# Kernel optimization log

Hardware: AMD Instinct MI355X
Metric: run time of the kernel (lower is better)

Reference implementation:

```python
import jax, jax.numpy as jnp
import numpy as np

B, T, E, WIN, OC, VOCAB = 256, 2048, 128, 5, 128, 50000


def setup_inputs() -> dict:
    key = jax.random.key(0)
    k1, k2, k3, k4, k5, k6 = jax.random.split(key, 6)
    return {
        "x": jax.random.randint(k1, (B, T), 0, VOCAB + 1, dtype=jnp.int32),
        "emb_table": jax.random.normal(k2, (VOCAB + 1, E), dtype=jnp.float32),
        "att_w": jax.random.normal(k3, (WIN, E), dtype=jnp.float32) * 0.05,
        "att_b": jax.random.normal(k4, (1,), dtype=jnp.float32),
        "cnn_w": jax.random.normal(k5, (OC, E), dtype=jnp.float32) * 0.05,
        "cnn_b": jax.random.normal(k6, (OC,), dtype=jnp.float32),
    }


def reference(x, emb_table, att_w, att_b, cnn_w, cnn_b):
    win = att_w.shape[0]
    pad = (win - 1) // 2
    embed = emb_table[x]                                   # [B, T, E]
    x_pad = jnp.pad(embed, ((0, 0), (pad, pad), (0, 0)))
    T_ = embed.shape[1]
    # Sliding-window dot product over full embed dim (the degenerate Conv2d)
    s = jnp.zeros(embed.shape[:2], dtype=embed.dtype)      # [B, T]
    for k in range(win):
        s = s + jnp.einsum('bte,e->bt', x_pad[:, k:k + T_, :], att_w[k])
    scores = jax.nn.sigmoid(s + att_b[0])                  # [B, T]
    gated = embed * scores[:, :, None]                     # [B, T, E]
    feat = jnp.tanh(jnp.einsum('bte,oe->bto', gated, cnn_w) + cnn_b)  # [B, T, OC]
    out = jnp.max(feat, axis=1)                            # [B, OC] (maxpool over seq)
    return out[:, :, None, None]                           # [B, OC, 1, 1]
```

## Files before the change

kernel.cpp:

```cpp
#include <hip/hip_runtime.h>
#include <hip/hip_bf16.h>
#include <math.h>

#define B_   256
#define T_   2048
#define E_   128
#define WIN_ 5
#define PAD_ 2
#define OC_  128
#define VOCAB_MAX 50000
#define VOCAB1 50001
#define TT   64
#define REAL_ROWS (TT + WIN_ - 1)
#define ROWS 80
#define ASTR 136
#define DSTR 132
#define VROWS 64
#define BT   256

typedef __attribute__((ext_vector_type(8))) short short8;
typedef __attribute__((ext_vector_type(4))) float floatx4;
typedef __attribute__((ext_vector_type(4))) unsigned uintx4;

static __device__ __forceinline__ short f2bf(float f) {
    union { __hip_bfloat16 h; short s; } u;
    u.h = __float2bfloat16(f);
    return u.s;
}

__device__ __forceinline__ void atomicMaxFloat(float* addr, float v) {
    if (v >= 0.0f) atomicMax((int*)addr, __float_as_int(v));
    else           atomicMin((unsigned int*)addr, __float_as_uint(v));
}

__launch_bounds__(256, 3)
__global__ void build_tables(const float* __restrict__ emb,
                             const float* __restrict__ cnn_w,
                             const float* __restrict__ att_w,
                             unsigned char* __restrict__ D8,
                             float* __restrict__ r,
                             float* __restrict__ rs,
                             float* __restrict__ out) {
    __shared__ __align__(16) short sh_a[VROWS * ASTR];
    __shared__ __align__(16) float sh_df[VROWS * DSTR];
    __shared__ float sh_inv[VROWS];

    const int tid  = threadIdx.x;
    const int lane = tid & 63;
    const int w    = tid >> 6;
    const int l15  = lane & 15;
    const int quad = lane >> 4;
    const int v0   = blockIdx.x * VROWS;

    if (blockIdx.x < (B_ * OC_) / 256)
        out[blockIdx.x * 256 + tid] = -INFINITY;

    #pragma unroll
    for (int t = 0; t < 8; t++) {
        int i   = t * 256 + tid;
        int row = i >> 5, c4 = i & 31;
        int vr  = v0 + row; if (vr > VOCAB_MAX) vr = VOCAB_MAX;
        float4 v = *(const float4*)(emb + (size_t)vr * E_ + c4 * 4);
        short4 o; o.x = f2bf(v.x); o.y = f2bf(v.y); o.z = f2bf(v.z); o.w = f2bf(v.w);
        *(short4*)(&sh_a[row * ASTR + c4 * 4]) = o;
    }

    short8 Bf[2][4];
    #pragma unroll
    for (int j = 0; j < 2; j++)
        #pragma unroll
        for (int ks = 0; ks < 4; ks++) {
            const float4* p = (const float4*)(cnn_w + (size_t)(w * 32 + j * 16 + l15) * E_ + ks * 32 + quad * 8);
            float4 p0 = p[0], p1 = p[1];
            Bf[j][ks] = (short8){ f2bf(p0.x), f2bf(p0.y), f2bf(p0.z), f2bf(p0.w),
                                  f2bf(p1.x), f2bf(p1.y), f2bf(p1.z), f2bf(p1.w) };
        }

    short8 Ba[4];
    #pragma unroll
    for (int ks = 0; ks < 4; ks++) {
        short8 v = (short8){0,0,0,0,0,0,0,0};
        if (l15 < WIN_) {
            const float4* p = (const float4*)(att_w + (size_t)l15 * E_ + ks * 32 + quad * 8);
            float4 p0 = p[0], p1 = p[1];
            v = (short8){ f2bf(p0.x), f2bf(p0.y), f2bf(p0.z), f2bf(p0.w),
                          f2bf(p1.x), f2bf(p1.y), f2bf(p1.z), f2bf(p1.w) };
        }
        Ba[ks] = v;
    }
    __syncthreads();

    #pragma unroll
    for (int mt = 0; mt < 4; mt++) {
        short8 a[4];
        #pragma unroll
        for (int ks = 0; ks < 4; ks++)
            a[ks] = *(const short8*)(&sh_a[(mt * 16 + l15) * ASTR + ks * 32 + quad * 8]);
        #pragma unroll
        for (int j = 0; j < 2; j++) {
            floatx4 acc = (floatx4){0.f, 0.f, 0.f, 0.f};
            #pragma unroll
            for (int ks = 0; ks < 4; ks++)
                acc = __builtin_amdgcn_mfma_f32_16x16x32_bf16(a[ks], Bf[j][ks], acc, 0, 0, 0);
            #pragma unroll
            for (int rr = 0; rr < 4; rr++)
                sh_df[(mt * 16 + quad * 4 + rr) * DSTR + w * 32 + j * 16 + l15] = acc[rr];
        }
    }

    {
        short8 a[4];
        #pragma unroll
        for (int ks = 0; ks < 4; ks++)
            a[ks] = *(const short8*)(&sh_a[(w * 16 + l15) * ASTR + ks * 32 + quad * 8]);
        floatx4 acc = (floatx4){0.f, 0.f, 0.f, 0.f};
        #pragma unroll
        for (int ks = 0; ks < 4; ks++)
            acc = __builtin_amdgcn_mfma_f32_16x16x32_bf16(a[ks], Ba[ks], acc, 0, 0, 0);
        if (l15 < 8) {
            #pragma unroll
            for (int rr = 0; rr < 4; rr++) {
                int v = v0 + w * 16 + quad * 4 + rr;
                if (v <= VOCAB_MAX) r[(size_t)v * 8 + l15] = acc[rr];
            }
        }
    }
    __syncthreads();

    {
        int row = tid >> 2, seg = tid & 3;
        const float4* p = (const float4*)(&sh_df[row * DSTR + seg * 32]);
        float m = 0.f;
        #pragma unroll
        for (int k = 0; k < 8; k++) {
            float4 v = p[k];
            m = fmaxf(m, fmaxf(fmaxf(fabsf(v.x), fabsf(v.y)), fmaxf(fabsf(v.z), fabsf(v.w))));
        }
        m = fmaxf(m, __shfl_xor(m, 1));
        m = fmaxf(m, __shfl_xor(m, 2));
        if (seg == 0) {
            sh_inv[row] = (m > 0.f) ? 127.f / m : 0.f;
            int v = v0 + row;
            if (v <= VOCAB_MAX) rs[v] = m * (1.f / 127.f);
        }
    }
    __syncthreads();

    #pragma unroll
    for (int st = 0; st < 2; st++) {
        int idx = st * 256 + tid;
        int row = idx >> 3, c8 = idx & 7;
        float inv = sh_inv[row];
        const float* p = &sh_df[row * DSTR + c8 * 16];
        uintx4 outw;
        #pragma unroll
        for (int q = 0; q < 4; q++) {
            unsigned dw = 0;
            #pragma unroll
            for (int k = 0; k < 4; k++) {
                int qi = (int)rintf(p[q * 4 + k] * inv);
                dw |= ((unsigned)(qi & 0xFF)) << (k * 8);
            }
            outw[q] = dw;
        }
        int v = v0 + row;
        if (v <= VOCAB_MAX)
            *(uintx4*)(D8 + (size_t)v * OC_ + c8 * 16) = outw;
    }
}

__launch_bounds__(256, 4)
__global__ void score_max(const int* __restrict__ x,
                          const unsigned char* __restrict__ D8,
                          const float* __restrict__ r,
                          const float* __restrict__ rs,
                          const float* __restrict__ att_b_p,
                          const float* __restrict__ cnn_b,
                          float* __restrict__ out) {
    __shared__ int   sh_x[BT + 4];
    __shared__ float sh_rs[BT + 4];
    __shared__ float sh_rt[WIN_][BT + 8];
    __shared__ float sh_sc[BT];
    __shared__ float sh_red[4][128];

    const int tid  = threadIdx.x;
    const int lane = tid & 63;
    const int w    = tid >> 6;
    const int b    = blockIdx.y;
    const int t0   = blockIdx.x * BT;
    const int l7   = lane & 7;
    const int grp8 = lane >> 3;

    for (int i = tid; i < BT + 4; i += 256) {
        int t = t0 + i - PAD_;
        int v = (t >= 0 && t < T_) ? x[b * T_ + t] : -1;
        sh_x[i] = v;
        float4 r03 = make_float4(0.f, 0.f, 0.f, 0.f);
        float  r4  = 0.f, rsv = 0.f;
        if (v >= 0) {
            r03 = *(const float4*)(r + (size_t)v * 8);
            r4  = r[(size_t)v * 8 + 4];
            rsv = rs[v];
        }
        sh_rt[0][i] = r03.x; sh_rt[1][i] = r03.y; sh_rt[2][i] = r03.z;
        sh_rt[3][i] = r03.w; sh_rt[4][i] = r4;
        sh_rs[i] = rsv;
    }
    __syncthreads();

    const int base_t = w * 64;

    uintx4 u[8];
    #pragma unroll
    for (int j = 0; j < 8; j++) {
        int tok = base_t + j * 8 + grp8;
        int v   = sh_x[tok + PAD_];
        u[j]    = *(const uintx4*)(D8 + (size_t)v * OC_ + l7 * 16);
    }

    {
        const float attb = att_b_p[0];
        float s = attb;
        #pragma unroll
        for (int k = 0; k < WIN_; k++) s += sh_rt[k][tid + k];
        sh_sc[tid] = sh_rs[tid + PAD_] / (1.0f + __expf(-s));
    }
    __syncthreads();

    float mm[16];
    #pragma unroll
    for (int c = 0; c < 16; c++) mm[c] = -INFINITY;

    float sc8[8];
    #pragma unroll
    for (int j = 0; j < 8; j++) sc8[j] = sh_sc[base_t + j * 8 + grp8];

    #pragma unroll
    for (int j = 0; j < 8; j++) {
        #pragma unroll
        for (int q = 0; q < 4; q++) {
            unsigned dw = u[j][q];
            #pragma unroll
            for (int k = 0; k < 4; k++) {
                int val = ((int)dw << (24 - k * 8)) >> 24;
                mm[q * 4 + k] = fmaxf(mm[q * 4 + k], sc8[j] * (float)val);
            }
        }
    }

    #pragma unroll
    for (int c = 0; c < 16; c++) {
        mm[c] = fmaxf(mm[c], __shfl_xor(mm[c], 8));
        mm[c] = fmaxf(mm[c], __shfl_xor(mm[c], 16));
        mm[c] = fmaxf(mm[c], __shfl_xor(mm[c], 32));
    }
    if (grp8 == 0) {
        #pragma unroll
        for (int c = 0; c < 16; c++) sh_red[w][l7 * 16 + c] = mm[c];
    }
    __syncthreads();
    if (tid < 128) {
        float m = fmaxf(fmaxf(sh_red[0][tid], sh_red[1][tid]),
                        fmaxf(sh_red[2][tid], sh_red[3][tid]));
        atomicMaxFloat(&out[b * OC_ + tid], tanhf(m + cnn_b[tid]));
    }
}

__global__ void prep_small(const float* __restrict__ cnn_w, const float* __restrict__ att_w,
                           short* __restrict__ wsw, short* __restrict__ wsatt) {
    int i = blockIdx.x * 256 + threadIdx.x;
    if (i < OC_ * E_)  wsw[i]   = f2bf(cnn_w[i]);
    if (i < WIN_ * E_) wsatt[i] = f2bf(att_w[i]);
}

__launch_bounds__(256, 4)
__global__ void fallback_main(const int* __restrict__ x,
                              const float* __restrict__ emb,
                              const float* __restrict__ att_b_p,
                              const short* __restrict__ wsw,
                              const short* __restrict__ wsatt,
                              const float* __restrict__ cnn_b,
                              float* __restrict__ out) {
    __shared__ short sh_a[ROWS * ASTR];
    __shared__ short sh_att[16 * ASTR];
    __shared__ float sh_r[ROWS * 8];
    __shared__ float sh_score[TT];
    __shared__ int   sh_idx[8 * ROWS];

    const int tid  = threadIdx.x;
    const int lane = tid & 63;
    const int w    = tid >> 6;
    const int b    = blockIdx.y;
    const int t0   = blockIdx.x * (8 * TT);
    const int l15  = lane & 15;
    const int quad = lane >> 4;
    const int rbase = tid >> 4;
    const int c     = tid & 15;

    for (int i = tid; i < 8 * ROWS; i += 256) {
        int tile = i / ROWS, row = i - tile * ROWS;
        int t = t0 + tile * TT + row - PAD_;
        sh_idx[i] = (row < REAL_ROWS && t >= 0 && t < T_) ? x[b * T_ + t] : -1;
    }
    {
        int o = tid >> 4, cc = tid & 15;
        short8 v = (short8){0,0,0,0,0,0,0,0};
        if (o < WIN_) v = *(const short8*)(wsatt + o * E_ + cc * 8);
        *(short8*)(&sh_att[o * ASTR + cc * 8]) = v;
    }
    short8 Bf[2][4];
    #pragma unroll
    for (int j = 0; j < 2; j++)
        #pragma unroll
        for (int ks = 0; ks < 4; ks++)
            Bf[j][ks] = *(const short8*)(wsw + (size_t)(w * 32 + j * 16 + l15) * E_ + ks * 32 + quad * 8);
    __syncthreads();

    short8 g[5];
    #pragma unroll
    for (int k = 0; k < 5; k++) {
        int idx = sh_idx[rbase + 16 * k];
        short8 v = (short8){0,0,0,0,0,0,0,0};
        if (idx >= 0) {
            const float4* p = (const float4*)(emb + (size_t)idx * E_ + c * 8);
            float4 p0 = p[0], p1 = p[1];
            v = (short8){ f2bf(p0.x), f2bf(p0.y), f2bf(p0.z), f2bf(p0.w),
                          f2bf(p1.x), f2bf(p1.y), f2bf(p1.z), f2bf(p1.w) };
        }
        g[k] = v;
    }
    #pragma unroll
    for (int k = 0; k < 5; k++)
        *(short8*)(&sh_a[(rbase + 16 * k) * ASTR + c * 8]) = g[k];
    __syncthreads();

    const float attb = att_b_p[0];
    float mm[2] = { -INFINITY, -INFINITY };

    for (int it = 0; it < 8; it++) {
        for (int mt = w; mt < 5; mt += 4) {
            floatx4 acc = (floatx4){0.f, 0.f, 0.f, 0.f};
            #pragma unroll
            for (int ks = 0; ks < 4; ks++) {
                short8 a  = *(const short8*)(&sh_a[(mt * 16 + l15) * ASTR + ks * 32 + quad * 8]);
                short8 bs = *(const short8*)(&sh_att[l15 * ASTR + ks * 32 + quad * 8]);
                acc = __builtin_amdgcn_mfma_f32_16x16x32_bf16(a, bs, acc, 0, 0, 0);
            }
            if (l15 < 8) {
                #pragma unroll
                for (int r = 0; r < 4; r++)
                    sh_r[(mt * 16 + quad * 4 + r) * 8 + l15] = acc[r];
            }
        }
        __syncthreads();

        if (it + 1 < 8) {
            const int* idxp = &sh_idx[(it + 1) * ROWS];
            #pragma unroll
            for (int k = 0; k < 5; k++) {
                int idx = idxp[rbase + 16 * k];
                short8 v = (short8){0,0,0,0,0,0,0,0};
                if (idx >= 0) {
                    const float4* p = (const float4*)(emb + (size_t)idx * E_ + c * 8);
                    float4 p0 = p[0], p1 = p[1];
                    v = (short8){ f2bf(p0.x), f2bf(p0.y), f2bf(p0.z), f2bf(p0.w),
                                  f2bf(p1.x), f2bf(p1.y), f2bf(p1.z), f2bf(p1.w) };
                }
                g[k] = v;
            }
        }

        if (tid < TT) {
            float s = attb;
            #pragma unroll
            for (int k = 0; k < WIN_; k++) s += sh_r[(tid + k) * 8 + k];
            sh_score[tid] = 1.0f / (1.0f + __expf(-s));
        }

        floatx4 acc[4][2];
        #pragma unroll
        for (int i = 0; i < 4; i++)
            #pragma unroll
            for (int j = 0; j < 2; j++) acc[i][j] = (floatx4){0.f, 0.f, 0.f, 0.f};
        #pragma unroll
        for (int ks = 0; ks < 4; ks++) {
            int ko = ks * 32 + quad * 8;
            #pragma unroll
            for (int i = 0; i < 4; i++) {
                short8 ai = *(const short8*)(&sh_a[(PAD_ + i * 16 + l15) * ASTR + ko]);
                acc[i][0] = __builtin_amdgcn_mfma_f32_16x16x32_bf16(ai, Bf[0][ks], acc[i][0], 0, 0, 0);
                acc[i][1] = __builtin_amdgcn_mfma_f32_16x16x32_bf16(ai, Bf[1][ks], acc[i][1], 0, 0, 0);
            }
        }
        __syncthreads();

        #pragma unroll
        for (int i = 0; i < 4; i++) {
            #pragma unroll
            for (int r = 0; r < 4; r++) {
                float sc = sh_score[i * 16 + quad * 4 + r];
                mm[0] = fmaxf(mm[0], sc * acc[i][0][r]);
                mm[1] = fmaxf(mm[1], sc * acc[i][1][r]);
            }
        }

        if (it + 1 < 8) {
            #pragma unroll
            for (int k = 0; k < 5; k++)
                *(short8*)(&sh_a[(rbase + 16 * k) * ASTR + c * 8]) = g[k];
            __syncthreads();
        }
    }

    #pragma unroll
    for (int j = 0; j < 2; j++) {
        float m = mm[j];
        m = fmaxf(m, __shfl_xor(m, 16));
        m = fmaxf(m, __shfl_xor(m, 32));
        if (lane < 16) {
            int o = w * 32 + j * 16 + lane;
            atomicMaxFloat(&out[b * OC_ + o], tanhf(m + cnn_b[o]));
        }
    }
}

extern "C" void kernel_launch(void* const* d_in, const int* in_sizes, int n_in,
                              void* d_out, int out_size, void* d_ws, size_t ws_size,
                              hipStream_t stream) {
    const int*   x     = (const int*)d_in[0];
    const float* emb   = (const float*)d_in[1];
    const float* att_w = (const float*)d_in[2];
    const float* att_b = (const float*)d_in[3];
    const float* cnn_w = (const float*)d_in[4];
    const float* cnn_b = (const float*)d_in[5];
    float* out = (float*)d_out;

    const size_t d8_bytes = (size_t)VOCAB1 * OC_;
    const size_t r_bytes  = (size_t)VOCAB1 * 8 * 4;
    const size_t rs_bytes = (size_t)VOCAB1 * 4;
    const size_t need = d8_bytes + r_bytes + rs_bytes + 64;

    if (ws_size >= need) {
        unsigned char* D8 = (unsigned char*)d_ws;
        float* rt = (float*)(D8 + d8_bytes);
        float* rsp = (float*)((char*)d_ws + d8_bytes + r_bytes);
        build_tables<<<(VOCAB1 + VROWS - 1) / VROWS, 256, 0, stream>>>(emb, cnn_w, att_w, D8, rt, rsp, out);
        dim3 grid(T_ / BT, B_);
        score_max<<<grid, 256, 0, stream>>>(x, D8, rt, rsp, att_b, cnn_b, out);
    } else {
        hipMemsetAsync(d_out, 0xFF, (size_t)B_ * OC_ * sizeof(float), stream);
        short* ws_w   = (short*)d_ws;
        short* ws_att = ws_w + OC_ * E_;
        prep_small<<<16, 256, 0, stream>>>(cnn_w, att_w, ws_w, ws_att);
        dim3 grid(T_ / (8 * TT), B_);
        fallback_main<<<grid, 256, 0, stream>>>(x, emb, att_b, ws_w, ws_att, cnn_b, out);
    }
}
```

Before: 106.4 us.

## Pack per-token attention terms and scale into one 16-byte record; bias int8 codes

Replaces the separate float r[8] and rs tables with a single 16-byte record per vocab entry, holding the float scale and five bf16 attention partial sums. score_max then does one gather per token instead of two scattered loads. The int8 D8 codes are stored offset by 128, so decoding uses an unsigned byte extract plus an fma with a precomputed -128*scale bias instead of sign-extending shifts. The attention terms lose precision going from fp32 to bf16, which slightly perturbs the sigmoid gate values.

After: 105.3 us. Within noise of the previous version (-1.0%).

```diff
diff --git a/kernel.cpp b/kernel.cpp
--- a/kernel.cpp
+++ b/kernel.cpp
@@ -38,12 +38,13 @@
                              const float* __restrict__ cnn_w,
                              const float* __restrict__ att_w,
                              unsigned char* __restrict__ D8,
-                             float* __restrict__ r,
-                             float* __restrict__ rs,
+                             unsigned char* __restrict__ rrec,
                              float* __restrict__ out) {
     __shared__ __align__(16) short sh_a[VROWS * ASTR];
     __shared__ __align__(16) float sh_df[VROWS * DSTR];
+    __shared__ float sh_rf[VROWS * 8];
     __shared__ float sh_inv[VROWS];
+    __shared__ float sh_rs[VROWS];
 
     const int tid  = threadIdx.x;
     const int lane = tid & 63;
@@ -119,10 +120,8 @@
             acc = __builtin_amdgcn_mfma_f32_16x16x32_bf16(a[ks], Ba[ks], acc, 0, 0, 0);
         if (l15 < 8) {
             #pragma unroll
-            for (int rr = 0; rr < 4; rr++) {
-                int v = v0 + w * 16 + quad * 4 + rr;
-                if (v <= VOCAB_MAX) r[(size_t)v * 8 + l15] = acc[rr];
-            }
+            for (int rr = 0; rr < 4; rr++)
+                sh_rf[(w * 16 + quad * 4 + rr) * 8 + l15] = acc[rr];
         }
     }
     __syncthreads();
@@ -140,8 +139,7 @@
         m = fmaxf(m, __shfl_xor(m, 2));
         if (seg == 0) {
             sh_inv[row] = (m > 0.f) ? 127.f / m : 0.f;
-            int v = v0 + row;
-            if (v <= VOCAB_MAX) rs[v] = m * (1.f / 127.f);
+            sh_rs[row]  = m * (1.f / 127.f);
         }
     }
     __syncthreads();
@@ -158,7 +156,7 @@
             unsigned dw = 0;
             #pragma unroll
             for (int k = 0; k < 4; k++) {
-                int qi = (int)rintf(p[q * 4 + k] * inv);
+                int qi = (int)rintf(p[q * 4 + k] * inv) + 128;
                 dw |= ((unsigned)(qi & 0xFF)) << (k * 8);
             }
             outw[q] = dw;
@@ -167,13 +165,27 @@
         if (v <= VOCAB_MAX)
             *(uintx4*)(D8 + (size_t)v * OC_ + c8 * 16) = outw;
     }
+
+    if (tid < VROWS) {
+        int v = v0 + tid;
+        if (v <= VOCAB_MAX) {
+            const float* rp = &sh_rf[tid * 8];
+            uintx4 rec;
+            rec[0] = __float_as_uint(sh_rs[tid]);
+            rec[1] = (unsigned)(unsigned short)f2bf(rp[0]) |
+                     ((unsigned)(unsigned short)f2bf(rp[1]) << 16);
+            rec[2] = (unsigned)(unsigned short)f2bf(rp[2]) |
+                     ((unsigned)(unsigned short)f2bf(rp[3]) << 16);
+            rec[3] = (unsigned)(unsigned short)f2bf(rp[4]);
+            *(uintx4*)(rrec + (size_t)v * 16) = rec;
+        }
+    }
 }
 
 __launch_bounds__(256, 4)
 __global__ void score_max(const int* __restrict__ x,
                           const unsigned char* __restrict__ D8,
-                          const float* __restrict__ r,
-                          const float* __restrict__ rs,
+                          const unsigned char* __restrict__ rrec,
                           const float* __restrict__ att_b_p,
                           const float* __restrict__ cnn_b,
                           float* __restrict__ out) {
@@ -195,15 +207,18 @@
         int t = t0 + i - PAD_;
         int v = (t >= 0 && t < T_) ? x[b * T_ + t] : -1;
         sh_x[i] = v;
-        float4 r03 = make_float4(0.f, 0.f, 0.f, 0.f);
-        float  r4  = 0.f, rsv = 0.f;
+        float rsv = 0.f, t0f = 0.f, t1f = 0.f, t2f = 0.f, t3f = 0.f, t4f = 0.f;
         if (v >= 0) {
-            r03 = *(const float4*)(r + (size_t)v * 8);
-            r4  = r[(size_t)v * 8 + 4];
-            rsv = rs[v];
-        }
-        sh_rt[0][i] = r03.x; sh_rt[1][i] = r03.y; sh_rt[2][i] = r03.z;
-        sh_rt[3][i] = r03.w; sh_rt[4][i] = r4;
+            uintx4 rec = *(const uintx4*)(rrec + (size_t)v * 16);
+            rsv = __uint_as_float(rec[0]);
+            t0f = __uint_as_float(rec[1] << 16);
+            t1f = __uint_as_float(rec[1] & 0xFFFF0000u);
+            t2f = __uint_as_float(rec[2] << 16);
+            t3f = __uint_as_float(rec[2] & 0xFFFF0000u);
+            t4f = __uint_as_float(rec[3] << 16);
+        }
+        sh_rt[0][i] = t0f; sh_rt[1][i] = t1f; sh_rt[2][i] = t2f;
+        sh_rt[3][i] = t3f; sh_rt[4][i] = t4f;
         sh_rs[i] = rsv;
     }
     __syncthreads();
@@ -231,9 +246,12 @@
     #pragma unroll
     for (int c = 0; c < 16; c++) mm[c] = -INFINITY;
 
-    float sc8[8];
-    #pragma unroll
-    for (int j = 0; j < 8; j++) sc8[j] = sh_sc[base_t + j * 8 + grp8];
+    float sc8[8], nb8[8];
+    #pragma unroll
+    for (int j = 0; j < 8; j++) {
+        sc8[j] = sh_sc[base_t + j * 8 + grp8];
+        nb8[j] = -128.f * sc8[j];
+    }
 
     #pragma unroll
     for (int j = 0; j < 8; j++) {
@@ -242,8 +260,8 @@
             unsigned dw = u[j][q];
             #pragma unroll
             for (int k = 0; k < 4; k++) {
-                int val = ((int)dw << (24 - k * 8)) >> 24;
-                mm[q * 4 + k] = fmaxf(mm[q * 4 + k], sc8[j] * (float)val);
+                float val = (float)((dw >> (k * 8)) & 0xFFu);
+                mm[q * 4 + k] = fmaxf(mm[q * 4 + k], fmaf(sc8[j], val, nb8[j]));
             }
         }
     }
@@ -435,18 +453,16 @@
     const float* cnn_b = (const float*)d_in[5];
     float* out = (float*)d_out;
 
-    const size_t d8_bytes = (size_t)VOCAB1 * OC_;
-    const size_t r_bytes  = (size_t)VOCAB1 * 8 * 4;
-    const size_t rs_bytes = (size_t)VOCAB1 * 4;
-    const size_t need = d8_bytes + r_bytes + rs_bytes + 64;
+    const size_t d8_bytes  = (size_t)VOCAB1 * OC_;
+    const size_t rec_bytes = (size_t)VOCAB1 * 16;
+    const size_t need = d8_bytes + rec_bytes + 64;
 
     if (ws_size >= need) {
         unsigned char* D8 = (unsigned char*)d_ws;
-        float* rt = (float*)(D8 + d8_bytes);
-        float* rsp = (float*)((char*)d_ws + d8_bytes + r_bytes);
-        build_tables<<<(VOCAB1 + VROWS - 1) / VROWS, 256, 0, stream>>>(emb, cnn_w, att_w, D8, rt, rsp, out);
+        unsigned char* rr = D8 + d8_bytes;
+        build_tables<<<(VOCAB1 + VROWS - 1) / VROWS, 256, 0, stream>>>(emb, cnn_w, att_w, D8, rr, out);
         dim3 grid(T_ / BT, B_);
-        score_max<<<grid, 256, 0, stream>>>(x, D8, rt, rsp, att_b, cnn_b, out);
+        score_max<<<grid, 256, 0, stream>>>(x, D8, rr, att_b, cnn_b, out);
     } else {
         hipMemsetAsync(d_out, 0xFF, (size_t)B_ * OC_ * sizeof(float), stream);
         short* ws_w   = (short*)d_ws;
```
